# Kernel tuning notes

Measured on AMD Instinct MI355X. Metric: run time of the kernel, lower is better.

The kernel has to match this reference:

```python
import jax, jax.numpy as jnp
import numpy as np

LEAK = 0.5  # leaking_rate alpha


def setup_inputs() -> dict:
    key = jax.random.key(0)
    k1, k2, k3, k4 = jax.random.split(key, 4)
    T, B, I, D = 512, 64, 768, 2048
    batch = jax.random.normal(k1, (T, B, I), dtype=jnp.float32)          # [max_len, batch, input_dim]
    input_w = jax.random.uniform(k2, (D, I), jnp.float32, -1.0, 1.0)     # input_scaling = 1.0
    res_w = jax.random.normal(k3, (D, D), dtype=jnp.float32) / jnp.sqrt(D)  # reservoir matrix (spectral-norm-ish)
    bias = jax.random.uniform(k4, (D,), jnp.float32, -0.1, 0.1)          # bias_scaling = 0.1
    return {"batch": batch, "input_w": input_w, "res_w": res_w, "bias": bias}


def reference(batch, input_w, res_w, bias):
    # ESN reservoir recurrence:
    #   h_t = (1-alpha) h_{t-1} + alpha * tanh(u_t W_in^T + h_{t-1} W_res^T + b)
    T, B, _ = batch.shape
    D = res_w.shape[0]
    # Precompute the input projection for all timesteps at once: [T, B, D]
    proj = jnp.einsum('tbi,di->tbd', batch, input_w) + bias

    def step(h, p_t):
        x = p_t + h @ res_w.T
        h_new = (1.0 - LEAK) * h + LEAK * jnp.tanh(x)
        return h_new, h_new

    h0 = jnp.zeros((B, D), dtype=batch.dtype)
    _, states = jax.lax.scan(step, h0, proj)  # states: [T, B, D]
    return states.transpose(1, 0, 2)          # [B, T, D], as in torch _forward
```

## Files before the change

kernel.cpp:

```cpp
#include <hip/hip_runtime.h>
#include <cstdint>
#include <cstddef>


typedef _Float16 half8 __attribute__((ext_vector_type(8)));
typedef float floatx4 __attribute__((ext_vector_type(4)));

#define T_SEQ   512
#define NBATCH  64
#define IN_DIM  768
#define D_DIM   2048
#define KI_PROJ 24

static constexpr size_t WS_WINHI = 0;
static constexpr size_t WS_WINLO = 3145728;
static constexpr size_t WS_H16   = 2 * 3145728;
static constexpr size_t WS_BAR   = WS_H16 + 524288;

__global__ __launch_bounds__(256) void prep_kernel(const float* __restrict__ input_w,
                                                   char* __restrict__ ws) {
  const int bid = blockIdx.x;
  const int tid = threadIdx.x;
  if (bid < 6144) {
    const int flat = bid * 256 + tid;
    const int j    = flat & 7;
    const int lane = (flat >> 3) & 63;
    const int q    = flat >> 9;
    const int ntG  = q / 24;
    const int ki   = q - ntG * 24;
    const int n    = ntG * 16 + (lane & 15);
    const int k    = ki * 32 + ((lane >> 4) << 3) + j;
    const float wv = input_w[n * IN_DIM + k];
    const _Float16 hi = (_Float16)wv;
    const _Float16 lo = (_Float16)(wv - (float)hi);
    ((_Float16*)(ws + WS_WINHI))[flat] = hi;
    ((_Float16*)(ws + WS_WINLO))[flat] = lo;
  } else if (bid < 6144 + 128) {
    const int idx = (bid - 6144) * 256 + tid;
    ((float4*)(ws + WS_H16))[idx] = make_float4(0.f, 0.f, 0.f, 0.f);
  } else {
    ((unsigned*)(ws + WS_BAR))[tid] = 0u;
  }
}

__global__ __launch_bounds__(256) void proj_kernel(const float* __restrict__ batch,
                                                   const float* __restrict__ bias,
                                                   const char* __restrict__ ws,
                                                   float* __restrict__ out) {
  __shared__ alignas(16) _Float16 Bs[2][16][512];
  const _Float16* WinHi = (const _Float16*)(ws + WS_WINHI);
  const _Float16* WinLo = (const _Float16*)(ws + WS_WINLO);
  const int tid = threadIdx.x;
  const int w = tid >> 6, l = tid & 63;
  const int nb = blockIdx.x, mb = blockIdx.y;

  floatx4 acc[2][8] = {};

  auto stage = [&](int ki, int buf) {
    #pragma unroll
    for (int c = 0; c < 4; ++c) {
      const int slot = w * 4 + c;
      const int nt = slot >> 1;
      const _Float16* src = (slot & 1) ? WinLo : WinHi;
      const _Float16* g = src + ((size_t)((nb * 8 + nt) * KI_PROJ + ki) * 64 + l) * 8;
      __builtin_amdgcn_global_load_lds(
          (const __attribute__((address_space(1))) unsigned int*)g,
          (__attribute__((address_space(3))) unsigned int*)&Bs[buf][slot][0], 16, 0, 0);
    }
  };

  stage(0, 0);
  __syncthreads();

  #pragma unroll 1
  for (int ki = 0; ki < KI_PROJ; ++ki) {
    const int buf = ki & 1;
    if (ki + 1 < KI_PROJ) stage(ki + 1, buf ^ 1);

    half8 ahi[2], alo[2];
    #pragma unroll
    for (int mt = 0; mt < 2; ++mt) {
      const int m = mb * 128 + (w * 2 + mt) * 16 + (l & 15);
      const int kb = ki * 32 + ((l >> 4) << 3);
      const float4 a0 = *(const float4*)(batch + (size_t)m * IN_DIM + kb);
      const float4 a1 = *(const float4*)(batch + (size_t)m * IN_DIM + kb + 4);
      const float av[8] = {a0.x, a0.y, a0.z, a0.w, a1.x, a1.y, a1.z, a1.w};
      #pragma unroll
      for (int jj = 0; jj < 8; ++jj) {
        const _Float16 h = (_Float16)av[jj];
        ahi[mt][jj] = h;
        alo[mt][jj] = (_Float16)(av[jj] - (float)h);
      }
    }
    #pragma unroll
    for (int nt = 0; nt < 8; ++nt) {
      const half8 bhi = *(const half8*)&Bs[buf][nt * 2][l * 8];
      const half8 blo = *(const half8*)&Bs[buf][nt * 2 + 1][l * 8];
      #pragma unroll
      for (int mt = 0; mt < 2; ++mt) {
        acc[mt][nt] = __builtin_amdgcn_mfma_f32_16x16x32_f16(ahi[mt], bhi, acc[mt][nt], 0, 0, 0);
        acc[mt][nt] = __builtin_amdgcn_mfma_f32_16x16x32_f16(ahi[mt], blo, acc[mt][nt], 0, 0, 0);
        acc[mt][nt] = __builtin_amdgcn_mfma_f32_16x16x32_f16(alo[mt], bhi, acc[mt][nt], 0, 0, 0);
      }
    }
    __syncthreads();
  }

  #pragma unroll
  for (int mt = 0; mt < 2; ++mt) {
    #pragma unroll
    for (int nt = 0; nt < 8; ++nt) {
      const int n = nb * 128 + nt * 16 + (l & 15);
      const float bv = bias[n];
      #pragma unroll
      for (int r = 0; r < 4; ++r) {
        const int m = mb * 128 + (w * 2 + mt) * 16 + ((l >> 4) << 2) + r;
        const int b = m & 63, ts = m >> 6;
        out[((size_t)b * T_SEQ + ts) * D_DIM + n] = acc[mt][nt][r] + bv;
      }
    }
  }
}

__device__ __forceinline__ float fast_tanh(float x) {
  const float e = __expf(-2.f * fabsf(x));
  return copysignf((1.f - e) / (1.f + e), x);
}

template <int WAVES, int NT>
__global__ __launch_bounds__(WAVES * 64, 1) void recur_kernel(const float* __restrict__ res_w,
                                                              float* out, char* ws) {
  constexpr int COLS = NT * 16;
  constexpr int BPR = D_DIM / COLS;
  constexpr int KPW = 64 / WAVES;

  extern __shared__ char smem[];
  _Float16* Wlds = (_Float16*)smem;
  float* red = (float*)(smem + (size_t)NT * 64 * 512 * 2);
  float* h32 = red + WAVES * 16 * 33;

  _Float16* h16 = (_Float16*)(ws + WS_H16);
  unsigned* bar = (unsigned*)(ws + WS_BAR);

  const int bid = blockIdx.x;
  const int rep = bid & 3;
  const int colbase = (bid >> 2) * COLS;
  const int bbase = rep * 16;
  const int tid = threadIdx.x;
  const int w = tid >> 6, l = tid & 63;

  for (int idx = tid; idx < COLS * D_DIM; idx += WAVES * 64) {
    const int dloc = idx >> 11;
    const int k = idx & 2047;
    const float wv = res_w[(size_t)(colbase + dloc) * D_DIM + k];
    const int lane = ((k >> 3) & 3) * 16 + (dloc & 15);
    Wlds[(((size_t)(dloc >> 4) * 64 + (k >> 5)) * 64 + lane) * 8 + (k & 7)] = (_Float16)wv;
  }
  if constexpr (WAVES > 1) {
    for (int idx = tid; idx < 16 * COLS; idx += WAVES * 64) h32[idx] = 0.f;
  }
  float hp0 = 0.f, hp1 = 0.f, hp2 = 0.f, hp3 = 0.f;
  __syncthreads();

  for (int t = 0; t < T_SEQ; ++t) {
    if (t > 0) {
      if (tid == 0) {
        const unsigned target = (unsigned)BPR * (unsigned)t;
        while (__hip_atomic_load(&bar[rep * 64], __ATOMIC_RELAXED, __HIP_MEMORY_SCOPE_AGENT) < target)
          __builtin_amdgcn_s_sleep(8);
      }
      __syncthreads();
      __builtin_amdgcn_fence(__ATOMIC_ACQUIRE, "agent");
    }

    const _Float16* hr = h16 + (size_t)((t + 1) & 1) * (NBATCH * D_DIM);
    const _Float16* hrow = hr + (size_t)(bbase + (l & 15)) * D_DIM + ((l >> 4) << 3);

    floatx4 acc[NT] = {};
    const int ki0 = w * KPW;
    #pragma unroll 4
    for (int kk = 0; kk < KPW; ++kk) {
      const int ki = ki0 + kk;
      const half8 a = *(const half8*)(hrow + ki * 32);
      #pragma unroll
      for (int nt = 0; nt < NT; ++nt) {
        const half8 bf = *(const half8*)&Wlds[(((size_t)nt * 64 + ki) * 64 + l) * 8];
        acc[nt] = __builtin_amdgcn_mfma_f32_16x16x32_f16(a, bf, acc[nt], 0, 0, 0);
      }
    }

    if constexpr (WAVES > 1) {
      #pragma unroll
      for (int nt = 0; nt < NT; ++nt)
        #pragma unroll
        for (int r = 0; r < 4; ++r)
          red[(w * 16 + ((l >> 4) << 2) + r) * 33 + nt * 16 + (l & 15)] = acc[nt][r];
      __syncthreads();
      const int n = tid & 31;
      const int m0 = tid >> 5;
      #pragma unroll
      for (int mm = 0; mm < 2; ++mm) {
        const int m = m0 + mm * 8;
        float x = red[(0 * 16 + m) * 33 + n] + red[(1 * 16 + m) * 33 + n] +
                  red[(2 * 16 + m) * 33 + n] + red[(3 * 16 + m) * 33 + n];
        const size_t gidx = ((size_t)(bbase + m) * T_SEQ + t) * D_DIM + colbase + n;
        x += out[gidx];
        const float hn = 0.5f * h32[m * COLS + n] + 0.5f * fast_tanh(x);
        h32[m * COLS + n] = hn;
        out[gidx] = hn;
        h16[(size_t)(t & 1) * (NBATCH * D_DIM) + (size_t)(bbase + m) * D_DIM + colbase + n] =
            (_Float16)hn;
      }
    } else {
      float hp[4] = {hp0, hp1, hp2, hp3};
      #pragma unroll
      for (int r = 0; r < 4; ++r) {
        const int m = ((l >> 4) << 2) + r;
        const int n = l & 15;
        const size_t gidx = ((size_t)(bbase + m) * T_SEQ + t) * D_DIM + colbase + n;
        const float x = acc[0][r] + out[gidx];
        const float hn = 0.5f * hp[r] + 0.5f * fast_tanh(x);
        hp[r] = hn;
        out[gidx] = hn;
        h16[(size_t)(t & 1) * (NBATCH * D_DIM) + (size_t)(bbase + m) * D_DIM + colbase + n] =
            (_Float16)hn;
      }
      hp0 = hp[0]; hp1 = hp[1]; hp2 = hp[2]; hp3 = hp[3];
    }

    __syncthreads();
    if (tid == 0)
      __hip_atomic_fetch_add(&bar[rep * 64], 1u, __ATOMIC_RELEASE, __HIP_MEMORY_SCOPE_AGENT);
  }
}

extern "C" void kernel_launch(void* const* d_in, const int* in_sizes, int n_in,
                              void* d_out, int out_size, void* d_ws, size_t ws_size,
                              hipStream_t stream) {
  const float* batch   = (const float*)d_in[0];
  const float* input_w = (const float*)d_in[1];
  const float* res_w   = (const float*)d_in[2];
  const float* bias    = (const float*)d_in[3];
  float* out = (float*)d_out;
  char* ws = (char*)d_ws;
  (void)in_sizes; (void)n_in; (void)out_size; (void)ws_size;

  prep_kernel<<<6273, 256, 0, stream>>>(input_w, ws);
  proj_kernel<<<dim3(16, 256), 256, 0, stream>>>(batch, bias, ws, out);

  int dev = 0;
  (void)hipGetDevice(&dev);
  int maxShmem = 0;
  (void)hipDeviceGetAttribute(&maxShmem, hipDeviceAttributeMaxSharedMemoryPerBlock, dev);
  constexpr size_t LDS_A = (size_t)2 * 64 * 512 * 2 + 4 * 16 * 33 * 4 + 16 * 32 * 4;
  if ((size_t)maxShmem >= LDS_A) {
    recur_kernel<4, 2><<<256, 256, LDS_A, stream>>>(res_w, out, ws);
  } else {
    recur_kernel<1, 1><<<512, 64, 65536, stream>>>(res_w, out, ws);
  }
}
```

Baseline: 9.987 ms.

## Replace atomic counter barrier with per-block flags and prefetch projection before wait

```diff
diff --git a/kernel.cpp b/kernel.cpp
--- a/kernel.cpp
+++ b/kernel.cpp
@@ -35,11 +35,13 @@
     const _Float16 lo = (_Float16)(wv - (float)hi);
     ((_Float16*)(ws + WS_WINHI))[flat] = hi;
     ((_Float16*)(ws + WS_WINLO))[flat] = lo;
-  } else if (bid < 6144 + 128) {
+  } else if (bid < 6272) {
     const int idx = (bid - 6144) * 256 + tid;
     ((float4*)(ws + WS_H16))[idx] = make_float4(0.f, 0.f, 0.f, 0.f);
   } else {
-    ((unsigned*)(ws + WS_BAR))[tid] = 0u;
+    uint4* p = (uint4*)(ws + WS_BAR);
+    #pragma unroll
+    for (int i = 0; i < 8; ++i) p[tid + i * 256] = make_uint4(0u, 0u, 0u, 0u);
   }
 }
 
@@ -163,11 +165,38 @@
   __syncthreads();
 
   for (int t = 0; t < T_SEQ; ++t) {
+    float pj[4];
+    size_t pg[4];
+    if constexpr (WAVES > 1) {
+      const int n_e = tid & 31;
+      const int m_e = tid >> 5;
+      pg[0] = ((size_t)(bbase + m_e) * T_SEQ + t) * D_DIM + colbase + n_e;
+      pg[1] = ((size_t)(bbase + m_e + 8) * T_SEQ + t) * D_DIM + colbase + n_e;
+      pj[0] = __builtin_nontemporal_load(out + pg[0]);
+      pj[1] = __builtin_nontemporal_load(out + pg[1]);
+    } else {
+      #pragma unroll
+      for (int r = 0; r < 4; ++r) {
+        const int m = ((l >> 4) << 2) + r;
+        pg[r] = ((size_t)(bbase + m) * T_SEQ + t) * D_DIM + colbase + (l & 15);
+        pj[r] = __builtin_nontemporal_load(out + pg[r]);
+      }
+    }
+
     if (t > 0) {
-      if (tid == 0) {
-        const unsigned target = (unsigned)BPR * (unsigned)t;
-        while (__hip_atomic_load(&bar[rep * 64], __ATOMIC_RELAXED, __HIP_MEMORY_SCOPE_AGENT) < target)
-          __builtin_amdgcn_s_sleep(8);
+      if (w == 0) {
+        bool ready;
+        do {
+          unsigned mn = 0xffffffffu;
+          #pragma unroll
+          for (int i = 0; i < BPR / 64; ++i) {
+            const int peer = rep + (l + i * 64) * 4;
+            const unsigned v = __hip_atomic_load(&bar[(size_t)peer * 16],
+                                                 __ATOMIC_RELAXED, __HIP_MEMORY_SCOPE_AGENT);
+            mn = v < mn ? v : mn;
+          }
+          ready = __all(mn >= (unsigned)t);
+        } while (!ready);
       }
       __syncthreads();
       __builtin_amdgcn_fence(__ATOMIC_ACQUIRE, "agent");
@@ -178,7 +207,7 @@
 
     floatx4 acc[NT] = {};
     const int ki0 = w * KPW;
-    #pragma unroll 4
+    #pragma unroll 16
     for (int kk = 0; kk < KPW; ++kk) {
       const int ki = ki0 + kk;
       const half8 a = *(const half8*)(hrow + ki * 32);
@@ -188,6 +217,8 @@
         acc[nt] = __builtin_amdgcn_mfma_f32_16x16x32_f16(a, bf, acc[nt], 0, 0, 0);
       }
     }
+
+    _Float16* hw = h16 + (size_t)(t & 1) * (NBATCH * D_DIM);
 
     if constexpr (WAVES > 1) {
       #pragma unroll
@@ -203,13 +234,11 @@
         const int m = m0 + mm * 8;
         float x = red[(0 * 16 + m) * 33 + n] + red[(1 * 16 + m) * 33 + n] +
                   red[(2 * 16 + m) * 33 + n] + red[(3 * 16 + m) * 33 + n];
-        const size_t gidx = ((size_t)(bbase + m) * T_SEQ + t) * D_DIM + colbase + n;
-        x += out[gidx];
+        x += pj[mm];
         const float hn = 0.5f * h32[m * COLS + n] + 0.5f * fast_tanh(x);
         h32[m * COLS + n] = hn;
-        out[gidx] = hn;
-        h16[(size_t)(t & 1) * (NBATCH * D_DIM) + (size_t)(bbase + m) * D_DIM + colbase + n] =
-            (_Float16)hn;
+        __builtin_nontemporal_store(hn, out + pg[mm]);
+        hw[(size_t)(bbase + m) * D_DIM + colbase + n] = (_Float16)hn;
       }
     } else {
       float hp[4] = {hp0, hp1, hp2, hp3};
@@ -217,20 +246,19 @@
       for (int r = 0; r < 4; ++r) {
         const int m = ((l >> 4) << 2) + r;
         const int n = l & 15;
-        const size_t gidx = ((size_t)(bbase + m) * T_SEQ + t) * D_DIM + colbase + n;
-        const float x = acc[0][r] + out[gidx];
+        const float x = acc[0][r] + pj[r];
         const float hn = 0.5f * hp[r] + 0.5f * fast_tanh(x);
         hp[r] = hn;
-        out[gidx] = hn;
-        h16[(size_t)(t & 1) * (NBATCH * D_DIM) + (size_t)(bbase + m) * D_DIM + colbase + n] =
-            (_Float16)hn;
+        __builtin_nontemporal_store(hn, out + pg[r]);
+        hw[(size_t)(bbase + m) * D_DIM + colbase + n] = (_Float16)hn;
       }
       hp0 = hp[0]; hp1 = hp[1]; hp2 = hp[2]; hp3 = hp[3];
     }
 
     __syncthreads();
     if (tid == 0)
-      __hip_atomic_fetch_add(&bar[rep * 64], 1u, __ATOMIC_RELEASE, __HIP_MEMORY_SCOPE_AGENT);
+      __hip_atomic_store(&bar[(size_t)bid * 16], (unsigned)(t + 1),
+                         __ATOMIC_RELEASE, __HIP_MEMORY_SCOPE_AGENT);
   }
 }
 
```

Measured after the change: 9.029 ms. 1.11x faster.
